# Kernel tuning notes

Hardware: AMD Instinct MI355X
Metric: run time of the kernel (lower is better)

## Reference

```python
import jax, jax.numpy as jnp
import numpy as np

NQ, BS, HW, D, H, DFF = 300, 16, 2048, 256, 8, 2048
HD2 = (2 * D) // H   # cross-attn head dim (query/key), 64
VHD = D // H         # value head dim, 32
EPS = 1e-5


def _lin_params(key, din, dout):
    kw, kb = jax.random.split(key)
    w = jax.random.normal(kw, (din, dout), jnp.float32) * 0.02
    b = jax.random.normal(kb, (dout,), jnp.float32) * 0.02
    return w, b


def setup_inputs() -> dict:
    key = jax.random.key(0)
    ks = jax.random.split(key, 24)
    inp = {
        'tgt': jax.random.normal(ks[0], (NQ, BS, D), jnp.float32),
        'memory': jax.random.normal(ks[1], (HW, BS, D), jnp.float32),
        'pos': jax.random.normal(ks[2], (HW, BS, D), jnp.float32),
        'cls_query_pos': jax.random.normal(ks[3], (NQ, BS, D), jnp.float32),
        'cls_query_sine_embed': jax.random.normal(ks[4], (NQ, BS, D), jnp.float32),
    }
    names = [('w_qc', 'b_qc', D, D), ('w_qp', 'b_qp', D, D), ('w_kc', 'b_kc', D, D),
             ('w_kp', 'b_kp', D, D), ('w_v', 'b_v', D, D), ('w_qs', 'b_qs', D, D),
             ('wq', 'bq', 2 * D, 2 * D), ('wk', 'bk', 2 * D, 2 * D),
             ('wv', 'bv', D, D), ('wo', 'bo', D, D),
             ('w1', 'b1', D, DFF), ('w2', 'b2', DFF, D)]
    for i, (wn, bn, din, dout) in enumerate(names):
        w, b = _lin_params(ks[5 + i], din, dout)
        inp[wn], inp[bn] = w, b
    inp['g2'] = jnp.ones((D,), jnp.float32)
    inp['be2'] = jnp.zeros((D,), jnp.float32)
    inp['g3'] = jnp.ones((D,), jnp.float32)
    inp['be3'] = jnp.zeros((D,), jnp.float32)
    return inp


def _ln(x, g, b):
    m = x.mean(-1, keepdims=True)
    v = ((x - m) ** 2).mean(-1, keepdims=True)
    return (x - m) * jax.lax.rsqrt(v + EPS) * g + b


def reference(tgt, memory, pos, cls_query_pos, cls_query_sine_embed,
              w_qc, b_qc, w_qp, b_qp, w_kc, b_kc, w_kp, b_kp, w_v, b_v,
              w_qs, b_qs, wq, bq, wk, bk, wv, bv, wo, bo,
              w1, b1, w2, b2, g2, be2, g3, be3):
    nq, bs, d = tgt.shape
    hw = memory.shape[0]
    # conditional cross-attention projections (is_first=True path)
    q_content = tgt @ w_qc + b_qc
    k_content = memory @ w_kc + b_kc
    v_in = memory @ w_v + b_v
    k_pos = pos @ w_kp + b_kp
    q_pos = cls_query_pos @ w_qp + b_qp
    q = (q_content + q_pos).reshape(nq, bs, H, d // H)
    sine = (cls_query_sine_embed @ w_qs + b_qs).reshape(nq, bs, H, d // H)
    q = jnp.concatenate([q, sine], axis=3).reshape(nq, bs, 2 * d)
    k = (k_content + k_pos).reshape(hw, bs, H, d // H)
    kp = k_pos.reshape(hw, bs, H, d // H)
    k = jnp.concatenate([k, kp], axis=3).reshape(hw, bs, 2 * d)
    # MultiheadAttention(embed_dim=2d, nhead, vdim=d): internal q/k/v/out projs
    scale = 1.0 / jnp.sqrt(jnp.float32(HD2))
    qh = ((q @ wq + bq) * scale).reshape(nq, bs, H, HD2)
    kh = (k @ wk + bk).reshape(hw, bs, H, HD2)
    vh = (v_in @ wv + bv).reshape(hw, bs, H, VHD)
    logits = jnp.einsum('qbhd,kbhd->bhqk', qh, kh)
    attn = jax.nn.softmax(logits, axis=-1)              # [bs, H, nq, hw]
    ctx = jnp.einsum('bhqk,kbhd->qbhd', attn, vh).reshape(nq, bs, d)
    tgt2 = ctx @ wo + bo
    attn_avg = attn.mean(axis=1)                        # averaged over heads
    # residual + norm + FFN + norm (dropout disabled / eval)
    x = _ln(tgt + tgt2, g2, be2)
    ffn = jax.nn.relu(x @ w1 + b1) @ w2 + b2
    x = _ln(x + ffn, g3, be3)
    return (x, attn_avg)
```

## Files before the change

### kernel.cpp

```cpp
#include <hip/hip_runtime.h>

typedef unsigned short u16;
typedef __attribute__((ext_vector_type(8))) short short8;
typedef __attribute__((ext_vector_type(4))) float f32x4;

#define MFMA16(a, b, c) __builtin_amdgcn_mfma_f32_16x16x32_bf16(a, b, c, 0, 0, 0)

__device__ __forceinline__ float bf2f(u16 u) {
    return __uint_as_float(((unsigned)u) << 16);
}
__device__ __forceinline__ u16 f2bf(float f) {
    unsigned u = __float_as_uint(f);
    u += 0x7fff + ((u >> 16) & 1);
    return (u16)(u >> 16);
}

__global__ __launch_bounds__(256) void cvt2(const float* __restrict__ a,
                                            const float* __restrict__ b,
                                            u16* __restrict__ A, u16* __restrict__ B) {
    size_t i = ((size_t)blockIdx.x * 256 + threadIdx.x) * 4;
    float4 va = *(const float4*)(a + i);
    float4 vb = *(const float4*)(b + i);
    u16 ta[4] = {f2bf(va.x), f2bf(va.y), f2bf(va.z), f2bf(va.w)};
    u16 tb[4] = {f2bf(vb.x), f2bf(vb.y), f2bf(vb.z), f2bf(vb.w)};
    *(uint2*)(A + i) = *(uint2*)ta;
    *(uint2*)(B + i) = *(uint2*)tb;
}


__global__ __launch_bounds__(256) void fold_q(const float* __restrict__ w_qc,
                                              const float* __restrict__ w_qp,
                                              const float* __restrict__ w_qs,
                                              const float* __restrict__ wq,
                                              u16* __restrict__ WQ3T) {
    int o = blockIdx.x * 256 + threadIdx.x;
    int k0 = blockIdx.y * 4;
    int seg = k0 >> 8, kb = k0 & 255;
    const float* wsrc = (seg == 0) ? w_qc : ((seg == 1) ? w_qp : w_qs);
    int sOff = (seg == 2) ? 32 : 0;
    const float* wcol = wq + o;
    float acc[4] = {0.f, 0.f, 0.f, 0.f};
#pragma unroll 8
    for (int c = 0; c < 256; c++) {
        int mc = (c >> 5) * 64 + (c & 31) + sOff;
        float w0 = wcol[(size_t)mc * 512];
#pragma unroll
        for (int j = 0; j < 4; j++)
            acc[j] += wsrc[(size_t)(kb + j) * 256 + c] * w0;
    }
    u16 outv[4];
#pragma unroll
    for (int j = 0; j < 4; j++) outv[j] = f2bf(acc[j] * 0.125f);
    *(uint2*)(WQ3T + (size_t)o * 768 + k0) = *(uint2*)outv;
}

__global__ __launch_bounds__(256) void fold_k(const float* __restrict__ w_kc,
                                              const float* __restrict__ w_kp,
                                              const float* __restrict__ wk,
                                              u16* __restrict__ WK2T) {
    int o = blockIdx.x * 256 + threadIdx.x;
    int k0 = blockIdx.y * 4;
    bool second = k0 >= 256;
    int kb = second ? k0 - 256 : k0;
    const float* wcol = wk + o;
    float acc[4] = {0.f, 0.f, 0.f, 0.f};
    if (second) {
#pragma unroll 8
        for (int c = 0; c < 256; c++) {
            int mc = (c >> 5) * 64 + (c & 31);
            float w0 = wcol[(size_t)mc * 512] + wcol[(size_t)(mc + 32) * 512];
#pragma unroll
            for (int j = 0; j < 4; j++)
                acc[j] += w_kp[(size_t)(kb + j) * 256 + c] * w0;
        }
    } else {
#pragma unroll 8
        for (int c = 0; c < 256; c++) {
            int mc = (c >> 5) * 64 + (c & 31);
            float w0 = wcol[(size_t)mc * 512];
#pragma unroll
            for (int j = 0; j < 4; j++)
                acc[j] += w_kc[(size_t)(kb + j) * 256 + c] * w0;
        }
    }
    u16 outv[4];
#pragma unroll
    for (int j = 0; j < 4; j++) outv[j] = f2bf(acc[j]);
    *(uint2*)(WK2T + (size_t)o * 512 + k0) = *(uint2*)outv;
}

__global__ __launch_bounds__(256) void fold_v(const float* __restrict__ w_v,
                                              const float* __restrict__ wv_w,
                                              u16* __restrict__ WV2T) {
    int o = threadIdx.x;
    int k0 = blockIdx.y * 4;
    float acc[4] = {0.f, 0.f, 0.f, 0.f};
#pragma unroll 8
    for (int c = 0; c < 256; c++) {
        float w0 = wv_w[(size_t)c * 256 + o];
#pragma unroll
        for (int j = 0; j < 4; j++)
            acc[j] += w_v[(size_t)(k0 + j) * 256 + c] * w0;
    }
    u16 outv[4];
#pragma unroll
    for (int j = 0; j < 4; j++) outv[j] = f2bf(acc[j]);
    *(uint2*)(WV2T + (size_t)o * 256 + k0) = *(uint2*)outv;
}

__global__ __launch_bounds__(256) void fold_bias(
    const float* b_qc, const float* b_qp, const float* b_qs, const float* wq, const float* bq,
    const float* b_kc, const float* b_kp, const float* wk, const float* bk,
    const float* b_v, const float* wv_w, const float* bv,
    float* BQF, float* BKF, float* BVF) {
    __shared__ float red[4][64];
    int tid = threadIdx.x, lane = tid & 63, wave = tid >> 6;
    int blk = blockIdx.x;
    float acc = 0.f;
    if (blk < 8) {
        int o = blk * 64 + lane;
#pragma unroll 4
        for (int c = wave * 64; c < wave * 64 + 64; c++) {
            int mc = (c >> 5) * 64 + (c & 31);
            acc += (b_qc[c] + b_qp[c]) * wq[(size_t)mc * 512 + o];
            acc += b_qs[c] * wq[(size_t)(mc + 32) * 512 + o];
        }
        red[wave][lane] = acc;
        __syncthreads();
        if (wave == 0)
            BQF[o] = (bq[o] + red[0][lane] + red[1][lane] + red[2][lane] + red[3][lane]) * 0.125f;
    } else if (blk < 16) {
        int o = (blk - 8) * 64 + lane;
#pragma unroll 4
        for (int c = wave * 64; c < wave * 64 + 64; c++) {
            int mc = (c >> 5) * 64 + (c & 31);
            acc += (b_kc[c] + b_kp[c]) * wk[(size_t)mc * 512 + o];
            acc += b_kp[c] * wk[(size_t)(mc + 32) * 512 + o];
        }
        red[wave][lane] = acc;
        __syncthreads();
        if (wave == 0)
            BKF[o] = bk[o] + red[0][lane] + red[1][lane] + red[2][lane] + red[3][lane];
    } else {
        int o = (blk - 16) * 64 + lane;
#pragma unroll 4
        for (int c = wave * 64; c < wave * 64 + 64; c++)
            acc += b_v[c] * wv_w[(size_t)c * 256 + o];
        red[wave][lane] = acc;
        __syncthreads();
        if (wave == 0)
            BVF[o] = bv[o] + red[0][lane] + red[1][lane] + red[2][lane] + red[3][lane];
    }
}

__global__ __launch_bounds__(256) void transpose_f2b(const float* __restrict__ src,
                                                     u16* __restrict__ dst, int R, int C) {
    __shared__ float tile[32][33];
    int c0 = blockIdx.x * 32, r0 = blockIdx.y * 32;
    int t = threadIdx.x;
    int j = t & 31, i0 = (t >> 5) * 4;
#pragma unroll
    for (int ii = 0; ii < 4; ii++)
        tile[i0 + ii][j] = src[(size_t)(r0 + i0 + ii) * C + c0 + j];
    __syncthreads();
    int i2 = t & 31, j0 = (t >> 5) * 4;
#pragma unroll
    for (int jj = 0; jj < 4; jj++)
        dst[(size_t)(c0 + j0 + jj) * R + r0 + i2] = f2bf(tile[i2][j0 + jj]);
}

#define APAD 40
__global__ __launch_bounds__(256) void gemm_bt(
    const void* __restrict__ A0v, const void* __restrict__ A1v, const void* __restrict__ A2v,
    int astride, int a_f32, const u16* __restrict__ BT, const float* __restrict__ bias,
    u16* __restrict__ C, int M, int N, int K, int mode) {
    __shared__ u16 As[128 * APAD];
    __shared__ u16 Bs[128 * APAD];
    int tid = threadIdx.x;
    int wave = tid >> 6, lane = tid & 63;
    int l15 = lane & 15, quad = lane >> 4;
    int wm = (wave >> 1) * 64, wn = (wave & 1) * 64;
    int gm0 = blockIdx.x * 128, gn0 = blockIdx.y * 128;
    f32x4 acc[4][4] = {};
    for (int k0 = 0; k0 < K; k0 += 32) {
        const void* ap;
        int kin;
        if (astride == 256) {
            int p = k0 >> 8;
            ap = (p == 0) ? A0v : ((p == 1) ? A1v : A2v);
            kin = k0 & 255;
        } else {
            ap = A0v;
            kin = k0;
        }
#pragma unroll
        for (int i = 0; i < 2; i++) {
            int idx = tid * 2 + i;
            int row = idx >> 2, seg = (idx & 3) * 8;
            int grow = gm0 + row;
            u16 tmp[8];
            if (a_f32) {
                float vv[8] = {0.f, 0.f, 0.f, 0.f, 0.f, 0.f, 0.f, 0.f};
                if (grow < M) {
                    const float* apf = (const float*)ap;
                    float4 u0 = *(const float4*)(apf + (size_t)grow * astride + kin + seg);
                    float4 u1 = *(const float4*)(apf + (size_t)grow * astride + kin + seg + 4);
                    vv[0] = u0.x; vv[1] = u0.y; vv[2] = u0.z; vv[3] = u0.w;
                    vv[4] = u1.x; vv[5] = u1.y; vv[6] = u1.z; vv[7] = u1.w;
                }
#pragma unroll
                for (int e = 0; e < 8; e++) tmp[e] = f2bf(vv[e]);
            } else {
                uint4 v;
                v.x = v.y = v.z = v.w = 0;
                if (grow < M) v = *(const uint4*)((const u16*)ap + (size_t)grow * astride + kin + seg);
                *(uint4*)tmp = v;
            }
            *(uint4*)(&As[row * APAD + seg]) = *(uint4*)tmp;
            int nrow = gn0 + row;
            uint4 w = *(const uint4*)(BT + (size_t)nrow * K + k0 + seg);
            *(uint4*)(&Bs[row * APAD + seg]) = w;
        }
        __syncthreads();
        short8 afr[4], bfr[4];
#pragma unroll
        for (int i = 0; i < 4; i++)
            afr[i] = *(const short8*)(&As[(wm + i * 16 + l15) * APAD + quad * 8]);
#pragma unroll
        for (int j = 0; j < 4; j++)
            bfr[j] = *(const short8*)(&Bs[(wn + j * 16 + l15) * APAD + quad * 8]);
#pragma unroll
        for (int i = 0; i < 4; i++)
#pragma unroll
            for (int j = 0; j < 4; j++) acc[i][j] = MFMA16(afr[i], bfr[j], acc[i][j]);
        __syncthreads();
    }
#pragma unroll
    for (int i = 0; i < 4; i++) {
        int row = gm0 + wm + i * 16 + quad * 4;
#pragma unroll
        for (int j = 0; j < 4; j++) {
            int col = gn0 + wn + j * 16 + l15;
            float bvv = bias[col];
#pragma unroll
            for (int r = 0; r < 4; r++) {
                int grow = row + r;
                if (grow < M) {
                    float v = acc[i][j][r] + bvv;
                    if (mode == 1) v = fmaxf(v, 0.f);
                    C[(size_t)grow * N + col] = f2bf(v);
                }
            }
        }
    }
}

__global__ __launch_bounds__(256) void transpose_v(const u16* __restrict__ vhr,
                                                   u16* __restrict__ vt) {
    int k0 = blockIdx.x * 128, b = blockIdx.y, h = blockIdx.z;
    int tid = threadIdx.x;
#pragma unroll
    for (int i = 0; i < 2; i++) {
        int idx = tid * 2 + i;
        int d = idx >> 4, ks = (idx & 15) * 8;
        u16 o[8];
#pragma unroll
        for (int e = 0; e < 8; e++)
            o[e] = vhr[((size_t)(k0 + ks + e) * 16 + b) * 256 + h * 32 + d];
        *(uint4*)(vt + ((size_t)(b * 8 + h) * 32 + d) * 2048 + k0 + ks) = *(uint4*)o;
    }
}

__global__ __launch_bounds__(256, 5) void attn_a(const u16* __restrict__ qh,
                                                 const u16* __restrict__ kh,
                                                 const u16* __restrict__ vt,
                                                 float* __restrict__ ctxp,
                                                 float* __restrict__ zp) {
    int l = blockIdx.x;
    int w = (l & 7) * 160 + (l >> 3);
    int g = w / 10;
    int iw = w - g * 10;
    int kc = iw / 5;
    int qt = iw - kc * 5;
    int h = g & 7, b = g >> 3;
    __shared__ u16 Kc[64 * 72];
    __shared__ u16 Pt[64 * 72];
    int tid = threadIdx.x, wave = tid >> 6, lane = tid & 63;
    int l15 = lane & 15, quad = lane >> 4;
    int q0 = qt * 64;
    int kb0 = kc * 1024;
    short8 qf[2];
    {
        short8 qz = {};
        qf[0] = qz;
        qf[1] = qz;
        int q = q0 + wave * 16 + l15;
        if (q < 300) {
            const u16* qp = qh + ((size_t)q * 16 + b) * 512 + h * 64 + quad * 8;
            qf[0] = *(const short8*)(qp);
            qf[1] = *(const short8*)(qp + 32);
        }
    }
    const u16* kbase = kh + (size_t)kb0 * 8192 + b * 512 + h * 64;
    const u16* vbase = vt + ((size_t)(b * 8 + h) * 32) * 2048 + kb0;
    f32x4 cacc[2] = {};
    float zl = 0.f;
    for (int it = 0; it < 16; ++it) {
#pragma unroll
        for (int i2 = 0; i2 < 2; i2++) {
            int idx = tid * 2 + i2;
            int row = idx >> 3, seg = (idx & 7) * 8;
            *(uint4*)(&Kc[row * 72 + seg]) =
                *(const uint4*)(kbase + (size_t)(it * 64 + row) * 8192 + seg);
        }
        __syncthreads();
        f32x4 sacc[4] = {};
#pragma unroll
        for (int d0 = 0; d0 < 2; d0++)
#pragma unroll
            for (int t = 0; t < 4; t++) {
                short8 af = *(const short8*)(&Kc[(t * 16 + l15) * 72 + d0 * 32 + quad * 8]);
                sacc[t] = MFMA16(af, qf[d0], sacc[t]);
            }
        __syncthreads();
#pragma unroll
        for (int t = 0; t < 4; t++) {
            u16 pk[4];
#pragma unroll
            for (int r = 0; r < 4; r++) {
                float p = __expf(sacc[t][r]);
                zl += p;
                pk[r] = f2bf(p);
            }
            *(uint2*)(&Pt[(wave * 16 + l15) * 72 + t * 16 + quad * 4]) = *(uint2*)pk;
        }
#pragma unroll
        for (int kk = 0; kk < 2; kk++) {
            short8 pa = *(const short8*)(&Pt[(wave * 16 + l15) * 72 + kk * 32 + quad * 8]);
#pragma unroll
            for (int t = 0; t < 2; t++) {
                short8 bf = *(const short8*)(vbase + (size_t)(t * 16 + l15) * 2048 +
                                             it * 64 + kk * 32 + quad * 8);
                cacc[t] = MFMA16(pa, bf, cacc[t]);
            }
        }
    }
    zl += __shfl_xor(zl, 16);
    zl += __shfl_xor(zl, 32);
    if (quad == 0) {
        int q = q0 + wave * 16 + l15;
        if (q < 300) zp[((size_t)kc * 128 + b * 8 + h) * 320 + q] = zl;
    }
    float* cp = ctxp + (size_t)kc * 5120 * 256;
#pragma unroll
    for (int r = 0; r < 4; r++) {
        int q = q0 + wave * 16 + quad * 4 + r;
        if (q < 300) {
#pragma unroll
            for (int t = 0; t < 2; t++)
                cp[((size_t)q * 16 + b) * 256 + h * 32 + t * 16 + l15] = cacc[t][r];
        }
    }
}

__global__ __launch_bounds__(256) void attn_norm(const float* __restrict__ ctxp,
                                                 const float* __restrict__ zp,
                                                 u16* __restrict__ ctx,
                                                 float* __restrict__ z8inv) {
    int row = blockIdx.x;
    int t = threadIdx.x;
    int q = row >> 4, b = row & 15;
    int h = t >> 5;
    float c = ctxp[(size_t)row * 256 + t] + ctxp[(size_t)5120 * 256 + (size_t)row * 256 + t];
    size_t zi = ((size_t)b * 8 + h) * 320 + q;
    float z = zp[zi] + zp[(size_t)128 * 320 + zi];
    float rz = 1.0f / z;
    ctx[(size_t)row * 256 + t] = f2bf(c * rz);
    if ((t & 31) == 0) z8inv[zi] = rz * 0.125f;
}

__global__ __launch_bounds__(256) void attn_b(const u16* __restrict__ qh,
                                              const u16* __restrict__ kh,
                                              const float* __restrict__ z8inv,
                                              float* __restrict__ out1) {
    int kc0 = blockIdx.x * 128, qt = blockIdx.y, b = blockIdx.z;
    __shared__ u16 Qt[64 * 72];
    __shared__ u16 Kc[128 * 72];
    int tid = threadIdx.x, wave = tid >> 6, lane = tid & 63;
    int l15 = lane & 15, quad = lane >> 4;
    int q0 = qt * 64;
    const f32x4 zf = {0.f, 0.f, 0.f, 0.f};
    float avg[8][4] = {};
    for (int h = 0; h < 8; h++) {
#pragma unroll
        for (int i = 0; i < 2; i++) {
            int idx = tid * 2 + i;
            int row = idx >> 3, seg = (idx & 7) * 8;
            uint4 v;
            v.x = v.y = v.z = v.w = 0;
            int q = q0 + row;
            if (q < 300) v = *(const uint4*)(qh + ((size_t)q * 16 + b) * 512 + h * 64 + seg);
            *(uint4*)(&Qt[row * 72 + seg]) = v;
        }
#pragma unroll
        for (int i = 0; i < 4; i++) {
            int idx = tid * 4 + i;
            int row = idx >> 3, seg = (idx & 7) * 8;
            *(uint4*)(&Kc[row * 72 + seg]) =
                *(const uint4*)(kh + ((size_t)(kc0 + row) * 16 + b) * 512 + h * 64 + seg);
        }
        __syncthreads();
        f32x4 sacc[8];
#pragma unroll
        for (int t = 0; t < 8; t++) sacc[t] = zf;
#pragma unroll
        for (int d0 = 0; d0 < 64; d0 += 32) {
            short8 af = *(const short8*)(&Qt[(wave * 16 + l15) * 72 + d0 + quad * 8]);
#pragma unroll
            for (int t = 0; t < 8; t++) {
                short8 bf = *(const short8*)(&Kc[(t * 16 + l15) * 72 + d0 + quad * 8]);
                sacc[t] = MFMA16(af, bf, sacc[t]);
            }
        }
        float zi[4];
#pragma unroll
        for (int r = 0; r < 4; r++) {
            int q = q0 + wave * 16 + quad * 4 + r;
            zi[r] = z8inv[((size_t)b * 8 + h) * 320 + (q < 319 ? q : 319)];
        }
#pragma unroll
        for (int t = 0; t < 8; t++)
#pragma unroll
            for (int r = 0; r < 4; r++) avg[t][r] += __expf(sacc[t][r]) * zi[r];
        __syncthreads();
    }
#pragma unroll
    for (int r = 0; r < 4; r++) {
        int q = q0 + wave * 16 + quad * 4 + r;
        if (q < 300) {
#pragma unroll
            for (int t = 0; t < 8; t++)
                out1[((size_t)b * 300 + q) * 2048 + kc0 + t * 16 + l15] = avg[t][r];
        }
    }
}

__global__ __launch_bounds__(256) void ln_kernel(const void* __restrict__ a, int a_f32,
                                                 const u16* __restrict__ bres,
                                                 const float* __restrict__ g,
                                                 const float* __restrict__ be,
                                                 void* __restrict__ out, int out_f32) {
    int row = blockIdx.x, t = threadIdx.x;
    float av = a_f32 ? ((const float*)a)[(size_t)row * 256 + t]
                     : bf2f(((const u16*)a)[(size_t)row * 256 + t]);
    float v = av + bf2f(bres[(size_t)row * 256 + t]);
    float s = v, sq = v * v;
#pragma unroll
    for (int o = 32; o; o >>= 1) {
        s += __shfl_xor(s, o);
        sq += __shfl_xor(sq, o);
    }
    __shared__ float red[8];
    int wave = t >> 6, lane = t & 63;
    if (lane == 0) {
        red[wave] = s;
        red[4 + wave] = sq;
    }
    __syncthreads();
    s = red[0] + red[1] + red[2] + red[3];
    sq = red[4] + red[5] + red[6] + red[7];
    float mean = s * (1.f / 256.f);
    float var = sq * (1.f / 256.f) - mean * mean;
    float rs = rsqrtf(var + 1e-5f);
    float res = (v - mean) * rs * g[t] + be[t];
    if (out_f32) ((float*)out)[(size_t)row * 256 + t] = res;
    else ((u16*)out)[(size_t)row * 256 + t] = f2bf(res);
}

extern "C" void kernel_launch(void* const* d_in, const int* in_sizes, int n_in,
                              void* d_out, int out_size, void* d_ws, size_t ws_size,
                              hipStream_t stream) {
    (void)in_sizes; (void)n_in; (void)out_size; (void)ws_size;
    const float* tgt = (const float*)d_in[0];
    const float* mem = (const float*)d_in[1];
    const float* pos = (const float*)d_in[2];
    const float* qpos = (const float*)d_in[3];
    const float* qsine = (const float*)d_in[4];
    const float* w_qc = (const float*)d_in[5];
    const float* b_qc = (const float*)d_in[6];
    const float* w_qp = (const float*)d_in[7];
    const float* b_qp = (const float*)d_in[8];
    const float* w_kc = (const float*)d_in[9];
    const float* b_kc = (const float*)d_in[10];
    const float* w_kp = (const float*)d_in[11];
    const float* b_kp = (const float*)d_in[12];
    const float* w_v = (const float*)d_in[13];
    const float* b_v = (const float*)d_in[14];
    const float* w_qs = (const float*)d_in[15];
    const float* b_qs = (const float*)d_in[16];
    const float* wq = (const float*)d_in[17];
    const float* bq = (const float*)d_in[18];
    const float* wk = (const float*)d_in[19];
    const float* bk = (const float*)d_in[20];
    const float* wv_w = (const float*)d_in[21];
    const float* bv = (const float*)d_in[22];
    const float* wo = (const float*)d_in[23];
    const float* bo = (const float*)d_in[24];
    const float* w1 = (const float*)d_in[25];
    const float* b1 = (const float*)d_in[26];
    const float* w2 = (const float*)d_in[27];
    const float* b2 = (const float*)d_in[28];
    const float* g2 = (const float*)d_in[29];
    const float* be2 = (const float*)d_in[30];
    const float* g3 = (const float*)d_in[31];
    const float* be3 = (const float*)d_in[32];

    char* ws = (char*)d_ws;
    u16* WQ3T = (u16*)(ws + 0x000000);
    u16* WK2T = (u16*)(ws + 0x0C0000);
    u16* WV2T = (u16*)(ws + 0x140000);
    u16* WOT  = (u16*)(ws + 0x160000);
    u16* W1T  = (u16*)(ws + 0x180000);
    u16* W2T  = (u16*)(ws + 0x280000);
    float* BQF = (float*)(ws + 0x380000);
    float* BKF = (float*)(ws + 0x381000);
    float* BVF = (float*)(ws + 0x382000);
    float* Z8  = (float*)(ws + 0x390000);
    u16* QH  = (u16*)(ws + 0x400000);
    u16* KH  = (u16*)(ws + 0x900000);
    u16* CTX = (u16*)(ws + 0x2900000);
    u16* TGT2 = (u16*)(ws + 0x900000);
    u16* XBUF = (u16*)(ws + 0xB60000);
    u16* FFNB = (u16*)(ws + 0xDC0000);
    u16* HBUF = (u16*)(ws + 0x1020000);

    float* out0 = (float*)d_out;
    float* out1 = out0 + 1228800;
    u16* MB  = (u16*)out1;
    u16* PB  = MB + 8388608;
    u16* VHR = PB;
    u16* VT  = MB;
    float* CTXP = (float*)PB;
    float* ZP   = CTXP + (size_t)2 * 5120 * 256;

    cvt2<<<8192, 256, 0, stream>>>(mem, pos, MB, PB);
    fold_q<<<dim3(2, 192), 256, 0, stream>>>(w_qc, w_qp, w_qs, wq, WQ3T);
    fold_k<<<dim3(2, 128), 256, 0, stream>>>(w_kc, w_kp, wk, WK2T);
    fold_v<<<dim3(1, 64), 256, 0, stream>>>(w_v, wv_w, WV2T);
    fold_bias<<<20, 256, 0, stream>>>(b_qc, b_qp, b_qs, wq, bq, b_kc, b_kp, wk, bk,
                                      b_v, wv_w, bv, BQF, BKF, BVF);
    transpose_f2b<<<dim3(8, 8), 256, 0, stream>>>(wo, WOT, 256, 256);
    transpose_f2b<<<dim3(64, 8), 256, 0, stream>>>(w1, W1T, 256, 2048);
    transpose_f2b<<<dim3(8, 64), 256, 0, stream>>>(w2, W2T, 2048, 256);

    gemm_bt<<<dim3(38, 4), 256, 0, stream>>>(tgt, qpos, qsine, 256, 1, WQ3T, BQF, QH, 4800, 512, 768, 0);
    gemm_bt<<<dim3(256, 4), 256, 0, stream>>>(MB, PB, nullptr, 256, 0, WK2T, BKF, KH, 32768, 512, 512, 0);
    gemm_bt<<<dim3(256, 2), 256, 0, stream>>>(MB, nullptr, nullptr, 256, 0, WV2T, BVF, VHR, 32768, 256, 256, 0);

    transpose_v<<<dim3(16, 16, 8), 256, 0, stream>>>(VHR, VT);
    attn_a<<<1280, 256, 0, stream>>>(QH, KH, VT, CTXP, ZP);
    attn_norm<<<4800, 256, 0, stream>>>(CTXP, ZP, CTX, Z8);
    attn_b<<<dim3(16, 5, 16), 256, 0, stream>>>(QH, KH, Z8, out1);

    gemm_bt<<<dim3(38, 2), 256, 0, stream>>>(CTX, nullptr, nullptr, 256, 0, WOT, bo, TGT2, 4800, 256, 256, 0);
    ln_kernel<<<4800, 256, 0, stream>>>(tgt, 1, TGT2, g2, be2, XBUF, 0);
    gemm_bt<<<dim3(38, 16), 256, 0, stream>>>(XBUF, nullptr, nullptr, 256, 0, W1T, b1, HBUF, 4800, 2048, 256, 1);
    gemm_bt<<<dim3(38, 2), 256, 0, stream>>>(HBUF, nullptr, nullptr, 2048, 0, W2T, b2, FFNB, 4800, 256, 2048, 0);
    ln_kernel<<<4800, 256, 0, stream>>>(XBUF, 0, FFNB, g3, be3, out0, 1);
}
```

Baseline: 588.5 us.

## Split-K the FFN down-projection and register-prefetch GEMM tiles

The GEMM kernel now loads the next K-slice of A and B into registers while MFMAs run on the current shared-memory tile, so global-load latency overlaps compute. It also supports split-K via gridDim.z. The FFN second GEMM (K=2048, only 76 blocks) now runs with two K halves writing fp32 partials, and the final layernorm sums the partials and adds the bias. This raises occupancy on the small-grid GEMM at the cost of extra fp32 partial traffic and higher register use from the prefetch buffers.

```diff
diff --git a/kernel.cpp b/kernel.cpp
--- a/kernel.cpp
+++ b/kernel.cpp
@@ -173,7 +173,7 @@
 __global__ __launch_bounds__(256) void gemm_bt(
     const void* __restrict__ A0v, const void* __restrict__ A1v, const void* __restrict__ A2v,
     int astride, int a_f32, const u16* __restrict__ BT, const float* __restrict__ bias,
-    u16* __restrict__ C, int M, int N, int K, int mode) {
+    void* __restrict__ Cv, void* __restrict__ C2v, int M, int N, int K, int mode) {
     __shared__ u16 As[128 * APAD];
     __shared__ u16 Bs[128 * APAD];
     int tid = threadIdx.x;
@@ -181,8 +181,14 @@
     int l15 = lane & 15, quad = lane >> 4;
     int wm = (wave >> 1) * 64, wn = (wave & 1) * 64;
     int gm0 = blockIdx.x * 128, gn0 = blockIdx.y * 128;
+    int kPer = K / gridDim.z;
+    int kStart = blockIdx.z * kPer, kEnd = kStart + kPer;
     f32x4 acc[4][4] = {};
-    for (int k0 = 0; k0 < K; k0 += 32) {
+    int row0 = (tid * 2) >> 2, seg0 = ((tid * 2) & 3) * 8;
+    int row1 = (tid * 2 + 1) >> 2, seg1 = ((tid * 2 + 1) & 3) * 8;
+    int growA0 = gm0 + row0, growA1 = gm0 + row1;
+    uint4 tA[2], tB[2];
+    auto LOAD = [&](int k0) {
         const void* ap;
         int kin;
         if (astride == 256) {
@@ -195,10 +201,8 @@
         }
 #pragma unroll
         for (int i = 0; i < 2; i++) {
-            int idx = tid * 2 + i;
-            int row = idx >> 2, seg = (idx & 3) * 8;
-            int grow = gm0 + row;
-            u16 tmp[8];
+            int row = i ? row1 : row0, seg = i ? seg1 : seg0;
+            int grow = i ? growA1 : growA0;
             if (a_f32) {
                 float vv[8] = {0.f, 0.f, 0.f, 0.f, 0.f, 0.f, 0.f, 0.f};
                 if (grow < M) {
@@ -208,20 +212,28 @@
                     vv[0] = u0.x; vv[1] = u0.y; vv[2] = u0.z; vv[3] = u0.w;
                     vv[4] = u1.x; vv[5] = u1.y; vv[6] = u1.z; vv[7] = u1.w;
                 }
+                u16 tmp[8];
 #pragma unroll
                 for (int e = 0; e < 8; e++) tmp[e] = f2bf(vv[e]);
+                tA[i] = *(uint4*)tmp;
             } else {
                 uint4 v;
                 v.x = v.y = v.z = v.w = 0;
                 if (grow < M) v = *(const uint4*)((const u16*)ap + (size_t)grow * astride + kin + seg);
-                *(uint4*)tmp = v;
+                tA[i] = v;
             }
-            *(uint4*)(&As[row * APAD + seg]) = *(uint4*)tmp;
             int nrow = gn0 + row;
-            uint4 w = *(const uint4*)(BT + (size_t)nrow * K + k0 + seg);
-            *(uint4*)(&Bs[row * APAD + seg]) = w;
-        }
-        __syncthreads();
+            tB[i] = *(const uint4*)(BT + (size_t)nrow * K + k0 + seg);
+        }
+    };
+    LOAD(kStart);
+    for (int k0 = kStart; k0 < kEnd; k0 += 32) {
+        *(uint4*)(&As[row0 * APAD + seg0]) = tA[0];
+        *(uint4*)(&Bs[row0 * APAD + seg0]) = tB[0];
+        *(uint4*)(&As[row1 * APAD + seg1]) = tA[1];
+        *(uint4*)(&Bs[row1 * APAD + seg1]) = tB[1];
+        __syncthreads();
+        if (k0 + 32 < kEnd) LOAD(k0 + 32);
         short8 afr[4], bfr[4];
 #pragma unroll
         for (int i = 0; i < 4; i++)
@@ -235,6 +247,24 @@
             for (int j = 0; j < 4; j++) acc[i][j] = MFMA16(afr[i], bfr[j], acc[i][j]);
         __syncthreads();
     }
+    if (mode == 2) {
+        float* Cf = (float*)(blockIdx.z == 0 ? Cv : C2v);
+#pragma unroll
+        for (int i = 0; i < 4; i++) {
+            int row = gm0 + wm + i * 16 + quad * 4;
+#pragma unroll
+            for (int j = 0; j < 4; j++) {
+                int col = gn0 + wn + j * 16 + l15;
+#pragma unroll
+                for (int r = 0; r < 4; r++) {
+                    int grow = row + r;
+                    if (grow < M) Cf[(size_t)grow * N + col] = acc[i][j][r];
+                }
+            }
+        }
+        return;
+    }
+    u16* C = (u16*)Cv;
 #pragma unroll
     for (int i = 0; i < 4; i++) {
         int row = gm0 + wm + i * 16 + quad * 4;
@@ -446,14 +476,21 @@
 }
 
 __global__ __launch_bounds__(256) void ln_kernel(const void* __restrict__ a, int a_f32,
-                                                 const u16* __restrict__ bres,
+                                                 const void* __restrict__ bres,
+                                                 const float* __restrict__ bres2,
+                                                 const float* __restrict__ badd,
                                                  const float* __restrict__ g,
                                                  const float* __restrict__ be,
                                                  void* __restrict__ out, int out_f32) {
     int row = blockIdx.x, t = threadIdx.x;
     float av = a_f32 ? ((const float*)a)[(size_t)row * 256 + t]
                      : bf2f(((const u16*)a)[(size_t)row * 256 + t]);
-    float v = av + bf2f(bres[(size_t)row * 256 + t]);
+    float bv;
+    if (bres2)
+        bv = ((const float*)bres)[(size_t)row * 256 + t] + bres2[(size_t)row * 256 + t] + badd[t];
+    else
+        bv = bf2f(((const u16*)bres)[(size_t)row * 256 + t]);
+    float v = av + bv;
     float s = v, sq = v * v;
 #pragma unroll
     for (int o = 32; o; o >>= 1) {
@@ -531,8 +568,9 @@
     u16* CTX = (u16*)(ws + 0x2900000);
     u16* TGT2 = (u16*)(ws + 0x900000);
     u16* XBUF = (u16*)(ws + 0xB60000);
-    u16* FFNB = (u16*)(ws + 0xDC0000);
     u16* HBUF = (u16*)(ws + 0x1020000);
+    float* FP0 = (float*)(ws + 0x400000);
+    float* FP1 = (float*)(ws + 0x22E0000);
 
     float* out0 = (float*)d_out;
     float* out1 = out0 + 1228800;
@@ -553,18 +591,18 @@
     transpose_f2b<<<dim3(64, 8), 256, 0, stream>>>(w1, W1T, 256, 2048);
     transpose_f2b<<<dim3(8, 64), 256, 0, stream>>>(w2, W2T, 2048, 256);
 
-    gemm_bt<<<dim3(38, 4), 256, 0, stream>>>(tgt, qpos, qsine, 256, 1, WQ3T, BQF, QH, 4800, 512, 768, 0);
-    gemm_bt<<<dim3(256, 4), 256, 0, stream>>>(MB, PB, nullptr, 256, 0, WK2T, BKF, KH, 32768, 512, 512, 0);
-    gemm_bt<<<dim3(256, 2), 256, 0, stream>>>(MB, nullptr, nullptr, 256, 0, WV2T, BVF, VHR, 32768, 256, 256, 0);
+    gemm_bt<<<dim3(38, 4), 256, 0, stream>>>(tgt, qpos, qsine, 256, 1, WQ3T, BQF, QH, nullptr, 4800, 512, 768, 0);
+    gemm_bt<<<dim3(256, 4), 256, 0, stream>>>(MB, PB, nullptr, 256, 0, WK2T, BKF, KH, nullptr, 32768, 512, 512, 0);
+    gemm_bt<<<dim3(256, 2), 256, 0, stream>>>(MB, nullptr, nullptr, 256, 0, WV2T, BVF, VHR, nullptr, 32768, 256, 256, 0);
 
     transpose_v<<<dim3(16, 16, 8), 256, 0, stream>>>(VHR, VT);
     attn_a<<<1280, 256, 0, stream>>>(QH, KH, VT, CTXP, ZP);
     attn_norm<<<4800, 256, 0, stream>>>(CTXP, ZP, CTX, Z8);
     attn_b<<<dim3(16, 5, 16), 256, 0, stream>>>(QH, KH, Z8, out1);
 
-    gemm_bt<<<dim3(38, 2), 256, 0, stream>>>(CTX, nullptr, nullptr, 256, 0, WOT, bo, TGT2, 4800, 256, 256, 0);
-    ln_kernel<<<4800, 256, 0, stream>>>(tgt, 1, TGT2, g2, be2, XBUF, 0);
-    gemm_bt<<<dim3(38, 16), 256, 0, stream>>>(XBUF, nullptr, nullptr, 256, 0, W1T, b1, HBUF, 4800, 2048, 256, 1);
-    gemm_bt<<<dim3(38, 2), 256, 0, stream>>>(HBUF, nullptr, nullptr, 2048, 0, W2T, b2, FFNB, 4800, 256, 2048, 0);
-    ln_kernel<<<4800, 256, 0, stream>>>(XBUF, 0, FFNB, g3, be3, out0, 1);
-}
+    gemm_bt<<<dim3(38, 2), 256, 0, stream>>>(CTX, nullptr, nullptr, 256, 0, WOT, bo, TGT2, nullptr, 4800, 256, 256, 0);
+    ln_kernel<<<4800, 256, 0, stream>>>(tgt, 1, TGT2, nullptr, nullptr, g2, be2, XBUF, 0);
+    gemm_bt<<<dim3(38, 16), 256, 0, stream>>>(XBUF, nullptr, nullptr, 256, 0, W1T, b1, HBUF, nullptr, 4800, 2048, 256, 1);
+    gemm_bt<<<dim3(38, 2, 2), 256, 0, stream>>>(HBUF, nullptr, nullptr, 2048, 0, W2T, b2, FP0, FP1, 4800, 256, 2048, 2);
+    ln_kernel<<<4800, 256, 0, stream>>>(XBUF, 0, FP0, FP1, b2, g3, be3, out0, 1);
+}
```

Result: slower. 1.014 ms (+72.3%).
